# Optimization experiments

Measured on AMD Instinct MI355X. Metric: run time of the kernel, lower is better.

The kernel has to match this reference:

```python
import jax, jax.numpy as jnp
import numpy as np

KERNEL_MUL = 2.0
KERNEL_NUM = 5
FIX_SIGMA = None


def setup_inputs() -> dict:
    key = jax.random.key(0)
    k1, k2 = jax.random.split(key)
    source = jax.random.normal(k1, (4096, 64), dtype=jnp.float32)
    target = jax.random.normal(k2, (4096, 64), dtype=jnp.float32)
    return {"source": source, "target": target}


def reference(source, target):
    batch_size = source.shape[0]
    total = jnp.concatenate([source, target], axis=0)  # [2N, D]
    n_samples = total.shape[0]
    sq = jnp.sum(total * total, axis=1)  # [2N]
    L2 = sq[:, None] + sq[None, :] - 2.0 * (total @ total.T)  # [2N, 2N]
    if FIX_SIGMA:
        bandwidth = jnp.asarray(FIX_SIGMA, dtype=L2.dtype)
    else:
        # torch uses L2_distance.data -> detached; no grad through bandwidth
        bandwidth = jax.lax.stop_gradient(jnp.sum(L2)) / (n_samples ** 2 - n_samples)
    bandwidth = bandwidth / (KERNEL_MUL ** (KERNEL_NUM // 2))
    kernels = jnp.zeros_like(L2)
    for i in range(KERNEL_NUM):  # small fixed loop over bandwidths
        kernels = kernels + jnp.exp(-L2 / (bandwidth * (KERNEL_MUL ** i)))
    XX = kernels[:batch_size, :batch_size]
    YY = kernels[batch_size:, batch_size:]
    XY = kernels[:batch_size, batch_size:]
    YX = kernels[batch_size:, :batch_size]
    return jnp.mean(XX + YY - XY - YX)
```

## Files before the change

### kernel.cpp

```cpp
#include <hip/hip_runtime.h>
#include <math.h>

#define N_TOTAL 8192
#define BATCH   4096
#define DIMS    64
#define P1_BLOCKS 512
#define SEG     8
#define P2_BLOCKS 1088


#if defined(__has_builtin)
#if __has_builtin(__builtin_amdgcn_exp2f)
#define EXP2F(x) __builtin_amdgcn_exp2f(x)
#endif
#endif
#ifndef EXP2F
#define EXP2F(x) exp2f(x)
#endif

typedef __attribute__((ext_vector_type(8))) short bf16x8;
typedef __attribute__((ext_vector_type(4))) float f32x4;
typedef __attribute__((ext_vector_type(2))) float f32x2;
typedef __attribute__((ext_vector_type(4))) short s16x4;

__device__ inline short f2bf_rn(float x) {
    unsigned u = __float_as_uint(x);
    unsigned r = (u + 0x7fffu + ((u >> 16) & 1u)) >> 16;
    return (short)r;
}

__global__ __launch_bounds__(256) void pass1_kernel(const float* __restrict__ src,
                                                    const float* __restrict__ tgt,
                                                    double* __restrict__ sqpart,
                                                    double* __restrict__ colpart,
                                                    float* __restrict__ sqbuf,
                                                    short* __restrict__ Xh) {
    __shared__ double cred[4][64];
    __shared__ double sred[4];
    const int lane = threadIdx.x & 63;
    const int wv = threadIdx.x >> 6;
    const int sub = lane >> 4;
    const int k4 = (lane & 15) << 2;
    const int gw = blockIdx.x * 4 + wv;
    const int numWaves = P1_BLOCKS * 4;

    double colacc[4] = {0.0, 0.0, 0.0, 0.0};
    double sqacc = 0.0;

    for (int g = gw; g < N_TOTAL / 4; g += numWaves) {
        int r = g * 4 + sub;
        const float* row = (r < BATCH) ? (src + (size_t)r * DIMS)
                                       : (tgt + (size_t)(r - BATCH) * DIMS);
        float4 v = *(const float4*)(row + k4);
        float xs[4] = {v.x, v.y, v.z, v.w};
        s16x4 h;
        float ssum = 0.f;
        #pragma unroll
        for (int i = 0; i < 4; ++i) {
            h[i] = f2bf_rn(xs[i]);
            colacc[i] += (double)xs[i];
            ssum = fmaf(xs[i], xs[i], ssum);
        }
        *(s16x4*)(Xh + (size_t)r * DIMS + k4) = h;
        ssum += __shfl_xor(ssum, 1, 64);
        ssum += __shfl_xor(ssum, 2, 64);
        ssum += __shfl_xor(ssum, 4, 64);
        ssum += __shfl_xor(ssum, 8, 64);
        if ((lane & 15) == 0) { sqbuf[r] = ssum; sqacc += (double)ssum; }
    }
    #pragma unroll
    for (int i = 0; i < 4; ++i) {
        colacc[i] += __shfl_xor(colacc[i], 16, 64);
        colacc[i] += __shfl_xor(colacc[i], 32, 64);
    }
    sqacc += __shfl_xor(sqacc, 16, 64);
    sqacc += __shfl_xor(sqacc, 32, 64);
    if (lane < 16) {
        #pragma unroll
        for (int i = 0; i < 4; ++i) cred[wv][lane * 4 + i] = colacc[i];
    }
    if (lane == 0) sred[wv] = sqacc;
    __syncthreads();
    if (wv == 0) {
        double c = (cred[0][lane] + cred[1][lane]) + (cred[2][lane] + cred[3][lane]);
        colpart[(size_t)blockIdx.x * 64 + lane] = c;
        if (lane == 0)
            sqpart[blockIdx.x] = (sred[0] + sred[1]) + (sred[2] + sred[3]);
    }
}

__global__ __launch_bounds__(512) void scale_kernel(const double* __restrict__ sqpart,
                                                    const double* __restrict__ colpart,
                                                    float* __restrict__ csp,
                                                    float* __restrict__ out) {
    __shared__ double cred[8][64];
    __shared__ double sred[8];
    const int t = threadIdx.x;
    const int lane = t & 63, w = t >> 6;
    if (t == 0) out[0] = 0.f;

    double colacc = 0.0;
    #pragma unroll 8
    for (int b = w; b < P1_BLOCKS; b += 8)
        colacc += colpart[(size_t)b * 64 + lane];
    cred[w][lane] = colacc;

    double sacc = sqpart[t];
    #pragma unroll
    for (int off = 32; off > 0; off >>= 1) sacc += __shfl_xor(sacc, off, 64);
    if (lane == 0) sred[w] = sacc;
    __syncthreads();

    if (w == 0) {
        double colsum = ((cred[0][lane] + cred[1][lane]) + (cred[2][lane] + cred[3][lane]))
                      + ((cred[4][lane] + cred[5][lane]) + (cred[6][lane] + cred[7][lane]));
        double vv = colsum * colsum;
        #pragma unroll
        for (int off = 32; off > 0; off >>= 1) vv += __shfl_xor(vv, off, 64);
        if (lane == 0) {
            double sq = ((sred[0] + sred[1]) + (sred[2] + sred[3]))
                      + ((sred[4] + sred[5]) + (sred[6] + sred[7]));
            const double n = (double)N_TOTAL;
            double bw0 = (2.0 * n * sq - 2.0 * vv) / (n * n - n) * 0.25;
            csp[0] = (float)(-1.0 / (bw0 * 0.6931471805599453 * 16.0));
        }
    }
}

__global__ __launch_bounds__(512) void pass2_kernel(const short* __restrict__ Xh,
                                                    const float* __restrict__ sqbuf,
                                                    const float* __restrict__ csp,
                                                    float* __restrict__ out) {
    const int f = blockIdx.x;
    int b = 0;
    while (4 * (b + 1) * (b + 2) <= f) ++b;
    const int rem = f - 4 * b * (b + 1);
    const int q = rem / (b + 1);
    const int bc = 8 * b + q;
    const int seg = rem - q * (b + 1);
    const int r0 = seg * SEG;
    const int r1 = (bc < r0 + SEG - 1) ? bc : r0 + SEG - 1;

    __shared__ __align__(16) short Bh[64][72];
    __shared__ float s_wred[8];

    const int t = threadIdx.x;
    const int lane = t & 63, w = t >> 6;
    const int strip = w & 3, ts = w >> 2;
    const int quad = lane >> 4, lrow = lane & 15;

    {
        int row = t >> 3;
        int c8 = (t & 7) << 3;
        size_t gsrc = (size_t)(bc * 64 + row) * DIMS + c8;
        *(s16x4*)&Bh[row][c8]     = *(const s16x4*)(Xh + gsrc);
        *(s16x4*)&Bh[row][c8 + 4] = *(const s16x4*)(Xh + gsrc + 4);
    }
    const float cs = csp[0];
    const float c2 = -2.f * cs;
    const f32x2 c2v = (f32x2){c2, c2};
    f32x2 sbj[4];
    #pragma unroll
    for (int j = 0; j < 4; ++j) {
        float s = sqbuf[bc * 64 + j * 16 + lrow] * cs;
        sbj[j] = (f32x2){s, s};
    }
    __syncthreads();

    const size_t aoff = (size_t)(strip * 16 + lrow) * DIMS + quad * 8;

    float facc = 0.f;

    for (int r = r0 + ts; r <= r1; r += 2) {
        const size_t abase = (size_t)r * 64 * DIMS + aoff;
        bf16x8 ah0 = *(const bf16x8*)(Xh + abase);
        bf16x8 ah1 = *(const bf16x8*)(Xh + abase + 32);
        float4 csa = *(const float4*)(sqbuf + r * 64 + strip * 16 + quad * 4);

        f32x4 acc[4];
        #pragma unroll
        for (int j = 0; j < 4; ++j) acc[j] = (f32x4){0.f, 0.f, 0.f, 0.f};
        #pragma unroll
        for (int j = 0; j < 4; ++j) {
            const int brow = j * 16 + lrow;
            const int bcol = quad * 8;
            bf16x8 bh0 = *(const bf16x8*)&Bh[brow][bcol];
            bf16x8 bh1 = *(const bf16x8*)&Bh[brow][bcol + 32];
            acc[j] = __builtin_amdgcn_mfma_f32_16x16x32_bf16(ah0, bh0, acc[j], 0, 0, 0);
            acc[j] = __builtin_amdgcn_mfma_f32_16x16x32_bf16(ah1, bh1, acc[j], 0, 0, 0);
        }

        const f32x2 sa01 = (f32x2){csa.x * cs, csa.y * cs};
        const f32x2 sa23 = (f32x2){csa.z * cs, csa.w * cs};
        f32x2 lsum2 = (f32x2){0.f, 0.f};
        #pragma unroll
        for (int j = 0; j < 4; ++j) {
            f32x2 a01 = (f32x2){acc[j][0], acc[j][1]};
            f32x2 a23 = (f32x2){acc[j][2], acc[j][3]};
            f32x2 t01 = a01 * c2v + (sa01 + sbj[j]);
            f32x2 t23 = a23 * c2v + (sa23 + sbj[j]);
            f32x2 e4a = (f32x2){EXP2F(t01[0]), EXP2F(t01[1])};
            f32x2 e4b = (f32x2){EXP2F(t23[0]), EXP2F(t23[1])};
            f32x2 e3a = e4a * e4a, e3b = e4b * e4b;
            f32x2 e2a = e3a * e3a, e2b = e3b * e3b;
            f32x2 e1a = e2a * e2a, e1b = e2b * e2b;
            f32x2 e0a = e1a * e1a, e0b = e1b * e1b;
            lsum2 += ((e0a + e1a) + (e2a + e3a)) + e4a;
            lsum2 += ((e0b + e1b) + (e2b + e3b)) + e4b;
        }
        float lsum = lsum2[0] + lsum2[1];
        float sgn = ((r < 64) == (bc < 64)) ? 1.f : -1.f;
        float wt  = (r == bc) ? 1.f : 2.f;
        facc = fmaf(lsum, sgn * wt, facc);
    }

    #pragma unroll
    for (int off = 32; off > 0; off >>= 1) facc += __shfl_xor(facc, off, 64);
    if (lane == 0) s_wred[w] = facc;
    __syncthreads();
    if (t == 0) {
        float bsum = ((s_wred[0] + s_wred[1]) + (s_wred[2] + s_wred[3]))
                   + ((s_wred[4] + s_wred[5]) + (s_wred[6] + s_wred[7]));
        atomicAdd(out, bsum * 5.9604644775390625e-08f);
    }
}

extern "C" void kernel_launch(void* const* d_in, const int* in_sizes, int n_in,
                              void* d_out, int out_size, void* d_ws, size_t ws_size,
                              hipStream_t stream) {
    const float* src = (const float*)d_in[0];
    const float* tgt = (const float*)d_in[1];
    char* ws = (char*)d_ws;
    double* sqpart  = (double*)ws;
    double* colpart = (double*)(ws + 4096);
    float*  csp     = (float*)(ws + 266240);
    float*  sqbuf   = (float*)(ws + 276480);
    short*  Xh      = (short*)(ws + 311296);


    pass1_kernel<<<P1_BLOCKS, 256, 0, stream>>>(src, tgt, sqpart, colpart,
                                                sqbuf, Xh);
    scale_kernel<<<1, 512, 0, stream>>>(sqpart, colpart, csp, (float*)d_out);

    pass2_kernel<<<P2_BLOCKS, 512, 0, stream>>>(Xh, sqbuf, csp, (float*)d_out);
}
```

Before: 82.66 us.

## Fold bandwidth reduction into pass2 and drop the separate scale kernel

Removes the single-block scale kernel. Every pass2 block now redundantly reduces the per-block column and square partials (pass1 shrunk to 128 blocks of 512 threads so there are fewer partials) to compute the bandwidth constant itself, and pass1 zeroes the output. This cuts one kernel launch and its serialization gap. In exchange each of the 1088 pass2 blocks adds about 64KB of partial-sum reads, an extra barrier and a small double-precision reduction.

Result: faster. 80.09 us (-3.1%).

```diff
diff --git a/kernel.cpp b/kernel.cpp
--- a/kernel.cpp
+++ b/kernel.cpp
@@ -4,7 +4,7 @@
 #define N_TOTAL 8192
 #define BATCH   4096
 #define DIMS    64
-#define P1_BLOCKS 512
+#define P1_BLOCKS 128
 #define SEG     8
 #define P2_BLOCKS 1088
 
@@ -29,20 +29,23 @@
     return (short)r;
 }
 
-__global__ __launch_bounds__(256) void pass1_kernel(const float* __restrict__ src,
+__global__ __launch_bounds__(512) void pass1_kernel(const float* __restrict__ src,
                                                     const float* __restrict__ tgt,
                                                     double* __restrict__ sqpart,
                                                     double* __restrict__ colpart,
                                                     float* __restrict__ sqbuf,
-                                                    short* __restrict__ Xh) {
-    __shared__ double cred[4][64];
-    __shared__ double sred[4];
+                                                    short* __restrict__ Xh,
+                                                    float* __restrict__ out) {
+    __shared__ double cred[8][64];
+    __shared__ double sred[8];
     const int lane = threadIdx.x & 63;
     const int wv = threadIdx.x >> 6;
     const int sub = lane >> 4;
     const int k4 = (lane & 15) << 2;
-    const int gw = blockIdx.x * 4 + wv;
-    const int numWaves = P1_BLOCKS * 4;
+    const int gw = blockIdx.x * 8 + wv;
+    const int numWaves = P1_BLOCKS * 8;
+
+    if (blockIdx.x == 0 && threadIdx.x == 0) out[0] = 0.f;
 
     double colacc[4] = {0.0, 0.0, 0.0, 0.0};
     double sqacc = 0.0;
@@ -82,54 +85,19 @@
     if (lane == 0) sred[wv] = sqacc;
     __syncthreads();
     if (wv == 0) {
-        double c = (cred[0][lane] + cred[1][lane]) + (cred[2][lane] + cred[3][lane]);
+        double c = ((cred[0][lane] + cred[1][lane]) + (cred[2][lane] + cred[3][lane]))
+                 + ((cred[4][lane] + cred[5][lane]) + (cred[6][lane] + cred[7][lane]));
         colpart[(size_t)blockIdx.x * 64 + lane] = c;
         if (lane == 0)
-            sqpart[blockIdx.x] = (sred[0] + sred[1]) + (sred[2] + sred[3]);
-    }
-}
-
-__global__ __launch_bounds__(512) void scale_kernel(const double* __restrict__ sqpart,
-                                                    const double* __restrict__ colpart,
-                                                    float* __restrict__ csp,
-                                                    float* __restrict__ out) {
-    __shared__ double cred[8][64];
-    __shared__ double sred[8];
-    const int t = threadIdx.x;
-    const int lane = t & 63, w = t >> 6;
-    if (t == 0) out[0] = 0.f;
-
-    double colacc = 0.0;
-    #pragma unroll 8
-    for (int b = w; b < P1_BLOCKS; b += 8)
-        colacc += colpart[(size_t)b * 64 + lane];
-    cred[w][lane] = colacc;
-
-    double sacc = sqpart[t];
-    #pragma unroll
-    for (int off = 32; off > 0; off >>= 1) sacc += __shfl_xor(sacc, off, 64);
-    if (lane == 0) sred[w] = sacc;
-    __syncthreads();
-
-    if (w == 0) {
-        double colsum = ((cred[0][lane] + cred[1][lane]) + (cred[2][lane] + cred[3][lane]))
-                      + ((cred[4][lane] + cred[5][lane]) + (cred[6][lane] + cred[7][lane]));
-        double vv = colsum * colsum;
-        #pragma unroll
-        for (int off = 32; off > 0; off >>= 1) vv += __shfl_xor(vv, off, 64);
-        if (lane == 0) {
-            double sq = ((sred[0] + sred[1]) + (sred[2] + sred[3]))
-                      + ((sred[4] + sred[5]) + (sred[6] + sred[7]));
-            const double n = (double)N_TOTAL;
-            double bw0 = (2.0 * n * sq - 2.0 * vv) / (n * n - n) * 0.25;
-            csp[0] = (float)(-1.0 / (bw0 * 0.6931471805599453 * 16.0));
-        }
+            sqpart[blockIdx.x] = ((sred[0] + sred[1]) + (sred[2] + sred[3]))
+                               + ((sred[4] + sred[5]) + (sred[6] + sred[7]));
     }
 }
 
 __global__ __launch_bounds__(512) void pass2_kernel(const short* __restrict__ Xh,
                                                     const float* __restrict__ sqbuf,
-                                                    const float* __restrict__ csp,
+                                                    const double* __restrict__ sqpart,
+                                                    const double* __restrict__ colpart,
                                                     float* __restrict__ out) {
     const int f = blockIdx.x;
     int b = 0;
@@ -142,7 +110,10 @@
     const int r1 = (bc < r0 + SEG - 1) ? bc : r0 + SEG - 1;
 
     __shared__ __align__(16) short Bh[64][72];
+    __shared__ double dcred[8][64];
+    __shared__ double s_sq[128];
     __shared__ float s_wred[8];
+    __shared__ float s_cs;
 
     const int t = threadIdx.x;
     const int lane = t & 63, w = t >> 6;
@@ -156,16 +127,51 @@
         *(s16x4*)&Bh[row][c8]     = *(const s16x4*)(Xh + gsrc);
         *(s16x4*)&Bh[row][c8 + 4] = *(const s16x4*)(Xh + gsrc + 4);
     }
-    const float cs = csp[0];
+
+    {
+        const int c = lane;
+        double colacc = 0.0;
+        #pragma unroll
+        for (int b2 = 0; b2 < P1_BLOCKS / 8; ++b2)
+            colacc += colpart[(size_t)(w + b2 * 8) * 64 + c];
+        dcred[w][c] = colacc;
+    }
+    if (t < 128) s_sq[t] = sqpart[t];
+
+    float sraw[4];
+    #pragma unroll
+    for (int j = 0; j < 4; ++j)
+        sraw[j] = sqbuf[bc * 64 + j * 16 + lrow];
+
+    __syncthreads();
+
+    if (w == 0) {
+        double colsum = ((dcred[0][lane] + dcred[1][lane]) + (dcred[2][lane] + dcred[3][lane]))
+                      + ((dcred[4][lane] + dcred[5][lane]) + (dcred[6][lane] + dcred[7][lane]));
+        double vv = colsum * colsum;
+        double sacc = s_sq[lane] + s_sq[lane + 64];
+        #pragma unroll
+        for (int off = 32; off > 0; off >>= 1) {
+            vv += __shfl_xor(vv, off, 64);
+            sacc += __shfl_xor(sacc, off, 64);
+        }
+        if (lane == 0) {
+            const double n = (double)N_TOTAL;
+            double bw0 = (2.0 * n * sacc - 2.0 * vv) / (n * n - n) * 0.25;
+            s_cs = (float)(-1.0 / (bw0 * 0.6931471805599453 * 16.0));
+        }
+    }
+    __syncthreads();
+
+    const float cs = s_cs;
     const float c2 = -2.f * cs;
     const f32x2 c2v = (f32x2){c2, c2};
     f32x2 sbj[4];
     #pragma unroll
     for (int j = 0; j < 4; ++j) {
-        float s = sqbuf[bc * 64 + j * 16 + lrow] * cs;
+        float s = sraw[j] * cs;
         sbj[j] = (f32x2){s, s};
     }
-    __syncthreads();
 
     const size_t aoff = (size_t)(strip * 16 + lrow) * DIMS + quad * 8;
 
@@ -232,15 +238,13 @@
     const float* tgt = (const float*)d_in[1];
     char* ws = (char*)d_ws;
     double* sqpart  = (double*)ws;
-    double* colpart = (double*)(ws + 4096);
-    float*  csp     = (float*)(ws + 266240);
-    float*  sqbuf   = (float*)(ws + 276480);
-    short*  Xh      = (short*)(ws + 311296);
-
-
-    pass1_kernel<<<P1_BLOCKS, 256, 0, stream>>>(src, tgt, sqpart, colpart,
-                                                sqbuf, Xh);
-    scale_kernel<<<1, 512, 0, stream>>>(sqpart, colpart, csp, (float*)d_out);
-
-    pass2_kernel<<<P2_BLOCKS, 512, 0, stream>>>(Xh, sqbuf, csp, (float*)d_out);
-}
+    double* colpart = (double*)(ws + 1024);
+    float*  sqbuf   = (float*)(ws + 66560);
+    short*  Xh      = (short*)(ws + 99328);
+
+
+    pass1_kernel<<<P1_BLOCKS, 512, 0, stream>>>(src, tgt, sqpart, colpart,
+                                                sqbuf, Xh, (float*)d_out);
+    pass2_kernel<<<P2_BLOCKS, 512, 0, stream>>>(Xh, sqbuf, sqpart, colpart,
+                                                (float*)d_out);
+}
```
